# Performance work log

Hardware: AMD Instinct MI355X
Metric: run time of the kernel (lower is better)

Reference implementation:

```python
import jax, jax.numpy as jnp
import numpy as np

def setup_inputs() -> dict:
    key = jax.random.key(0)
    k1, k2 = jax.random.split(key)
    B, T_enc, T_dec, D = 8, 2048, 2048, 512
    encoder_outputs = jax.random.normal(k1, (B, T_enc, D), dtype=jnp.float32)
    decoder_outputs = jax.random.normal(k2, (B, T_dec, D), dtype=jnp.float32)
    return {"encoder_outputs": encoder_outputs, "decoder_outputs": decoder_outputs}

def reference(encoder_outputs, decoder_outputs):
    # score[b,e,t] = sum_d enc[b,e,d] * dec[b,t,d]
    score = jnp.einsum('bed,btd->bet', encoder_outputs, decoder_outputs)
    # softmax over encoder-time axis (axis=-2)
    attn = jax.nn.softmax(score, axis=1)  # [B, T_enc, T_dec]
    # context[b,t,d] = sum_e enc[b,e,d] * attn[b,e,t]  (avoids 4D broadcast)
    context = jnp.einsum('bed,bet->btd', encoder_outputs, attn)
    return jnp.concatenate([decoder_outputs, context], axis=-1)  # [B, T_dec, 2D]
```

## Files before the change

### kernel.cpp

```cpp
#include <hip/hip_runtime.h>


typedef _Float16 f16;
typedef f16 f16x8 __attribute__((ext_vector_type(8)));
typedef f16 f16x4 __attribute__((ext_vector_type(4)));
typedef float f32x4 __attribute__((ext_vector_type(4)));

#define NB 8
#define TE 2048
#define TD 2048
#define DD 512
#define TBLK 64
#define EBLK 32
#define NCH (TE / EBLK)

#define OKHI 0
#define OKT  32768
#define OS4  73728
#define OP   92160
#define OPSZ 5120
#define OAL  102400
#define OLL  102912
#define OFLG 103168
#define SMEM_BYTES 103232

__device__ __forceinline__ int swz1k(int row, int byteInRow) {
    return row * 1024 + (byteInRow ^ ((row & 7) << 4));
}

__global__ __launch_bounds__(512, 2)
void attn_fused(const float* __restrict__ enc, const float* __restrict__ dec,
                float* __restrict__ out) {
    __shared__ __align__(16) char sm[SMEM_BYTES];
    const int tid  = threadIdx.x;
    const int b    = blockIdx.x & 7;
    const int t0   = (blockIdx.x >> 3) * TBLK;
    const int lane = tid & 63;
    const int wv   = tid >> 6;
    const int li   = lane & 15;
    const int gi   = lane >> 4;
    const int et   = wv & 1;
    const int kq   = wv >> 1;
    const float L2E = 1.44269504088896f;

    const float* encB = enc + (size_t)b * TE * DD;
    const float* decB = dec + (size_t)b * TD * DD;
    float*       outB = out + (size_t)b * TD * (2 * DD);

    const int c4 = tid & 127;
    const int rb = tid >> 7;

    f32x4 st[8];
    #pragma unroll
    for (int i = 0; i < 8; ++i)
        st[i] = *(const f32x4*)(encB + (size_t)(8 * rb + i) * DD + 4 * c4);

    f16x8 qF[4][4];
    #pragma unroll
    for (int kk = 0; kk < 4; ++kk)
        #pragma unroll
        for (int tl = 0; tl < 4; ++tl) {
            const float* qp = decB + (size_t)(t0 + 16 * tl + li) * DD
                            + 128 * kq + 32 * kk + 8 * gi;
            f32x4 q0 = *(const f32x4*)qp;
            f32x4 q1 = *(const f32x4*)(qp + 4);
            f16x8 h;
            #pragma unroll
            for (int j = 0; j < 4; ++j) { h[j] = (f16)q0[j]; h[4 + j] = (f16)q1[j]; }
            qF[kk][tl] = h;
        }

    f16x4 hvB[8];
    #pragma unroll
    for (int i = 0; i < 8; ++i) {
        f16x4 h4 = {(f16)st[i][0], (f16)st[i][1], (f16)st[i][2], (f16)st[i][3]};
        hvB[i] = h4;
        *(f16x4*)(sm + OKHI + swz1k(8 * rb + i, 8 * c4)) = h4;
    }
    #pragma unroll
    for (int i = 0; i < 8; ++i)
        st[i] = *(const f32x4*)(encB + (size_t)(EBLK + 8 * rb + i) * DD + 4 * c4);
    __syncthreads();

    const int cq   = lane & 7;
    const int erq  = lane >> 3;
    const int tcol = 8 * wv + cq;
    float mrun = -1.0e30f;
    float lpart = 0.0f;

    f32x4 ctx[4][4];
    #pragma unroll
    for (int md = 0; md < 4; ++md)
        #pragma unroll
        for (int tt = 0; tt < 4; ++tt)
            ctx[md][tt] = (f32x4){0.f, 0.f, 0.f, 0.f};

    for (int ch = 0; ch < NCH; ++ch) {
        const int pb = ch & 1;
        const int qb = pb ^ 1;
        const bool doPV = (ch > 0);
        const bool more = (ch + 1 < NCH);

        f32x4 sacc[4];
        #pragma unroll
        for (int tl = 0; tl < 4; ++tl)
            sacc[tl] = (f32x4){0.f, 0.f, 0.f, 0.f};
        __builtin_amdgcn_s_setprio(1);
        #pragma unroll
        for (int kk = 0; kk < 4; ++kk) {
            int cb = 256 * kq + 64 * kk + 16 * gi;
            f16x8 aF = *(const f16x8*)(sm + OKHI + swz1k(16 * et + li, cb));
            #pragma unroll
            for (int tl = 0; tl < 4; ++tl)
                sacc[tl] = __builtin_amdgcn_mfma_f32_16x16x32_f16(aF, qF[kk][tl], sacc[tl], 0, 0, 0);
        }
        __builtin_amdgcn_s_setprio(0);
        #pragma unroll
        for (int tl = 0; tl < 4; ++tl) {
            f16x4 sh = {(f16)sacc[tl][0], (f16)sacc[tl][1],
                        (f16)sacc[tl][2], (f16)sacc[tl][3]};
            *(f16x4*)(sm + OS4 + kq * 4608 + (16 * tl + li) * 72
                      + 32 * et + 8 * gi) = sh;
        }
        __syncthreads();

        f32x4 s4 = (f32x4){0.f, 0.f, 0.f, 0.f};
        #pragma unroll
        for (int bu = 0; bu < 4; ++bu) {
            f16x4 h = *(const f16x4*)(sm + OS4 + bu * 4608 + tcol * 72 + 8 * erq);
            #pragma unroll
            for (int j = 0; j < 4; ++j) s4[j] += (float)h[j];
        }

        bool doR = false;
        f16x8 bP[4];
        if (doPV) {
            const uint4* fp = (const uint4*)(sm + OFLG + 32 * qb);
            uint4 f0 = fp[0], f1 = fp[1];
            doR = (f0.x | f0.y | f0.z | f0.w | f1.x | f1.y | f1.z | f1.w) != 0;
            #pragma unroll
            for (int tt = 0; tt < 4; ++tt)
                bP[tt] = *(const f16x8*)(sm + OP + OPSZ * qb + (16 * tt + li) * 80 + 16 * gi);
        }
        {
            float pml = fmaxf(fmaxf(s4[0], s4[1]), fmaxf(s4[2], s4[3]));
            bool trip = pml > mrun + 8.0f;
            unsigned long long bal = __ballot(trip);
            float alpha = 1.0f;
            if (bal != 0ULL) {
                float pm = pml;
                pm = fmaxf(pm, __shfl_xor(pm, 8));
                pm = fmaxf(pm, __shfl_xor(pm, 16));
                pm = fmaxf(pm, __shfl_xor(pm, 32));
                float mnew = fmaxf(mrun, pm);
                alpha = exp2f((mrun - mnew) * L2E);
                lpart *= alpha;
                mrun = mnew;
            }
            f32x4 p4;
            #pragma unroll
            for (int j = 0; j < 4; ++j) p4[j] = exp2f((s4[j] - mrun) * L2E);
            lpart += p4[0] + p4[1] + p4[2] + p4[3];
            f16x4 pw = {(f16)p4[0], (f16)p4[1], (f16)p4[2], (f16)p4[3]};
            *(f16x4*)(sm + OP + OPSZ * pb + tcol * 80 + 8 * erq) = pw;
            if (erq == 0) *(float*)(sm + OAL + 256 * pb + 4 * tcol) = alpha;
            if (lane == 0) *(unsigned*)(sm + OFLG + 32 * pb + 4 * wv) = (bal != 0ULL) ? 1u : 0u;
        }
        if (doPV) {
            if (doR) {
                float av[4];
                #pragma unroll
                for (int tt = 0; tt < 4; ++tt)
                    av[tt] = *(const float*)(sm + OAL + 256 * qb + 4 * (16 * tt + li));
                #pragma unroll
                for (int md = 0; md < 4; ++md)
                    #pragma unroll
                    for (int tt = 0; tt < 4; ++tt)
                        #pragma unroll
                        for (int r = 0; r < 4; ++r) ctx[md][tt][r] *= av[tt];
            }
            __builtin_amdgcn_s_setprio(1);
            #pragma unroll
            for (int md = 0; md < 4; ++md) {
                int dv = 64 * wv + 16 * md + li;
                int sig = ((dv >> 3) & 3) << 4;
                f16x8 a = *(const f16x8*)(sm + OKT + dv * 80 + ((16 * gi) ^ sig));
                #pragma unroll
                for (int tt = 0; tt < 4; ++tt)
                    ctx[md][tt] = __builtin_amdgcn_mfma_f32_16x16x32_f16(a, bP[tt], ctx[md][tt], 0, 0, 0);
            }
            __builtin_amdgcn_s_setprio(0);
        }
        f16x4 hvA[8];
        if (more) {
            #pragma unroll
            for (int i = 0; i < 8; ++i) {
                f16x4 h4 = {(f16)st[i][0], (f16)st[i][1], (f16)st[i][2], (f16)st[i][3]};
                hvA[i] = h4;
                *(f16x4*)(sm + OKHI + swz1k(8 * rb + i, 8 * c4)) = h4;
            }
            if (ch + 2 < NCH) {
                const float* src = encB + (size_t)(ch + 2) * EBLK * DD;
                #pragma unroll
                for (int i = 0; i < 8; ++i)
                    st[i] = *(const f32x4*)(src + (size_t)(8 * rb + i) * DD + 4 * c4);
            }
        }
        __syncthreads();
        #pragma unroll
        for (int k = 0; k < 4; ++k) {
            int d = 4 * c4 + k;
            int sig = ((d >> 3) & 3) << 4;
            f16x8 q8 = {hvB[0][k], hvB[1][k], hvB[2][k], hvB[3][k],
                        hvB[4][k], hvB[5][k], hvB[6][k], hvB[7][k]};
            *(f16x8*)(sm + OKT + d * 80 + ((16 * rb) ^ sig)) = q8;
        }
        if (more) {
            #pragma unroll
            for (int i = 0; i < 8; ++i) hvB[i] = hvA[i];
        }
    }

    __syncthreads();

    {
        const int qb2 = (NCH - 1) & 1;
        const uint4* fp = (const uint4*)(sm + OFLG + 32 * qb2);
        uint4 f0 = fp[0], f1 = fp[1];
        bool doR = (f0.x | f0.y | f0.z | f0.w | f1.x | f1.y | f1.z | f1.w) != 0;
        f16x8 bP[4];
        #pragma unroll
        for (int tt = 0; tt < 4; ++tt)
            bP[tt] = *(const f16x8*)(sm + OP + OPSZ * qb2 + (16 * tt + li) * 80 + 16 * gi);
        if (doR) {
            float av[4];
            #pragma unroll
            for (int tt = 0; tt < 4; ++tt)
                av[tt] = *(const float*)(sm + OAL + 256 * qb2 + 4 * (16 * tt + li));
            #pragma unroll
            for (int md = 0; md < 4; ++md)
                #pragma unroll
                for (int tt = 0; tt < 4; ++tt)
                    #pragma unroll
                    for (int r = 0; r < 4; ++r) ctx[md][tt][r] *= av[tt];
        }
        #pragma unroll
        for (int md = 0; md < 4; ++md) {
            int dv = 64 * wv + 16 * md + li;
            int sig = ((dv >> 3) & 3) << 4;
            f16x8 a = *(const f16x8*)(sm + OKT + dv * 80 + ((16 * gi) ^ sig));
            #pragma unroll
            for (int tt = 0; tt < 4; ++tt)
                ctx[md][tt] = __builtin_amdgcn_mfma_f32_16x16x32_f16(a, bP[tt], ctx[md][tt], 0, 0, 0);
        }
    }

    {
        float ps = lpart;
        ps += __shfl_xor(ps, 8);
        ps += __shfl_xor(ps, 16);
        ps += __shfl_xor(ps, 32);
        if (erq == 0) *(float*)(sm + OLL + 4 * tcol) = ps;
    }
    __syncthreads();
    float inv[4];
    #pragma unroll
    for (int tt = 0; tt < 4; ++tt)
        inv[tt] = 1.0f / *(const float*)(sm + OLL + 4 * (16 * tt + li));
    #pragma unroll
    for (int md = 0; md < 4; ++md)
        #pragma unroll
        for (int tt = 0; tt < 4; ++tt) {
            int t = t0 + 16 * tt + li;
            int d = 64 * wv + 16 * md + 4 * gi;
            float4 o;
            o.x = ctx[md][tt][0] * inv[tt];
            o.y = ctx[md][tt][1] * inv[tt];
            o.z = ctx[md][tt][2] * inv[tt];
            o.w = ctx[md][tt][3] * inv[tt];
            *(float4*)(outB + (size_t)t * (2 * DD) + DD + d) = o;
        }
    #pragma unroll
    for (int it = 0; it < TBLK * (DD / 4) / 512; ++it) {
        int i = tid + it * 512;
        int t = i >> 7, cc = i & 127;
        float4 q = ((const float4*)(decB + (size_t)(t0 + t) * DD))[cc];
        ((float4*)(outB + (size_t)(t0 + t) * (2 * DD)))[cc] = q;
    }
}

extern "C" void kernel_launch(void* const* d_in, const int* in_sizes, int n_in,
                              void* d_out, int out_size, void* d_ws, size_t ws_size,
                              hipStream_t stream) {
    const float* enc = (const float*)d_in[0];
    const float* dec = (const float*)d_in[1];
    float* out = (float*)d_out;
    dim3 grid(NB * (TD / TBLK));
    dim3 block(512);
    attn_fused<<<grid, block, 0, stream>>>(enc, dec, out);
}
```

Measured before the change: 132.9 us.

## Software-pipeline softmax of previous chunk against current chunk's QK MFMAs

Double-buffers the shared-memory score staging area. Each iteration now reduces and exponentiates the scores of the previous chunk while the QK^T MFMAs for the current chunk run, instead of waiting on a barrier between the score write and the softmax. The last chunk's softmax and PV move into a longer epilogue with an extra barrier. LDS use grows by about 18 KB, which may reduce occupancy and adds register pressure from the prefetched score fragments.

```diff
diff --git a/kernel.cpp b/kernel.cpp
--- a/kernel.cpp
+++ b/kernel.cpp
@@ -17,12 +17,13 @@
 #define OKHI 0
 #define OKT  32768
 #define OS4  73728
-#define OP   92160
+#define OS4SZ 18432
+#define OP   110592
 #define OPSZ 5120
-#define OAL  102400
-#define OLL  102912
-#define OFLG 103168
-#define SMEM_BYTES 103232
+#define OAL  120832
+#define OLL  121344
+#define OFLG 121600
+#define SMEM_BYTES 121664
 
 __device__ __forceinline__ int swz1k(int row, int byteInRow) {
     return row * 1024 + (byteInRow ^ ((row & 7) << 4));
@@ -97,10 +98,16 @@
 
     for (int ch = 0; ch < NCH; ++ch) {
         const int pb = ch & 1;
-        const int qb = pb ^ 1;
-        const bool doPV = (ch > 0);
+        const int sp = (ch + 1) & 1;
+        const bool doSM = (ch > 0);
         const bool more = (ch + 1 < NCH);
 
+        f16x4 sh4[4];
+        if (doSM) {
+            #pragma unroll
+            for (int bu = 0; bu < 4; ++bu)
+                sh4[bu] = *(const f16x4*)(sm + OS4 + OS4SZ * sp + bu * 4608 + tcol * 72 + 8 * erq);
+        }
         f32x4 sacc[4];
         #pragma unroll
         for (int tl = 0; tl < 4; ++tl)
@@ -115,34 +122,12 @@
                 sacc[tl] = __builtin_amdgcn_mfma_f32_16x16x32_f16(aF, qF[kk][tl], sacc[tl], 0, 0, 0);
         }
         __builtin_amdgcn_s_setprio(0);
-        #pragma unroll
-        for (int tl = 0; tl < 4; ++tl) {
-            f16x4 sh = {(f16)sacc[tl][0], (f16)sacc[tl][1],
-                        (f16)sacc[tl][2], (f16)sacc[tl][3]};
-            *(f16x4*)(sm + OS4 + kq * 4608 + (16 * tl + li) * 72
-                      + 32 * et + 8 * gi) = sh;
-        }
-        __syncthreads();
-
-        f32x4 s4 = (f32x4){0.f, 0.f, 0.f, 0.f};
-        #pragma unroll
-        for (int bu = 0; bu < 4; ++bu) {
-            f16x4 h = *(const f16x4*)(sm + OS4 + bu * 4608 + tcol * 72 + 8 * erq);
-            #pragma unroll
-            for (int j = 0; j < 4; ++j) s4[j] += (float)h[j];
-        }
-
-        bool doR = false;
-        f16x8 bP[4];
-        if (doPV) {
-            const uint4* fp = (const uint4*)(sm + OFLG + 32 * qb);
-            uint4 f0 = fp[0], f1 = fp[1];
-            doR = (f0.x | f0.y | f0.z | f0.w | f1.x | f1.y | f1.z | f1.w) != 0;
-            #pragma unroll
-            for (int tt = 0; tt < 4; ++tt)
-                bP[tt] = *(const f16x8*)(sm + OP + OPSZ * qb + (16 * tt + li) * 80 + 16 * gi);
-        }
-        {
+        if (doSM) {
+            f32x4 s4 = (f32x4){0.f, 0.f, 0.f, 0.f};
+            #pragma unroll
+            for (int bu = 0; bu < 4; ++bu)
+                #pragma unroll
+                for (int j = 0; j < 4; ++j) s4[j] += (float)sh4[bu][j];
             float pml = fmaxf(fmaxf(s4[0], s4[1]), fmaxf(s4[2], s4[3]));
             bool trip = pml > mrun + 8.0f;
             unsigned long long bal = __ballot(trip);
@@ -162,16 +147,32 @@
             for (int j = 0; j < 4; ++j) p4[j] = exp2f((s4[j] - mrun) * L2E);
             lpart += p4[0] + p4[1] + p4[2] + p4[3];
             f16x4 pw = {(f16)p4[0], (f16)p4[1], (f16)p4[2], (f16)p4[3]};
-            *(f16x4*)(sm + OP + OPSZ * pb + tcol * 80 + 8 * erq) = pw;
-            if (erq == 0) *(float*)(sm + OAL + 256 * pb + 4 * tcol) = alpha;
-            if (lane == 0) *(unsigned*)(sm + OFLG + 32 * pb + 4 * wv) = (bal != 0ULL) ? 1u : 0u;
-        }
-        if (doPV) {
+            *(f16x4*)(sm + OP + OPSZ * sp + tcol * 80 + 8 * erq) = pw;
+            if (erq == 0) *(float*)(sm + OAL + 256 * sp + 4 * tcol) = alpha;
+            if (lane == 0) *(unsigned*)(sm + OFLG + 32 * sp + 4 * wv) = (bal != 0ULL) ? 1u : 0u;
+        }
+        #pragma unroll
+        for (int tl = 0; tl < 4; ++tl) {
+            f16x4 sh = {(f16)sacc[tl][0], (f16)sacc[tl][1],
+                        (f16)sacc[tl][2], (f16)sacc[tl][3]};
+            *(f16x4*)(sm + OS4 + OS4SZ * pb + kq * 4608 + (16 * tl + li) * 72
+                      + 32 * et + 8 * gi) = sh;
+        }
+        __syncthreads();
+
+        if (doSM) {
+            const uint4* fp = (const uint4*)(sm + OFLG + 32 * sp);
+            uint4 f0 = fp[0], f1 = fp[1];
+            bool doR = (f0.x | f0.y | f0.z | f0.w | f1.x | f1.y | f1.z | f1.w) != 0;
+            f16x8 bP[4];
+            #pragma unroll
+            for (int tt = 0; tt < 4; ++tt)
+                bP[tt] = *(const f16x8*)(sm + OP + OPSZ * sp + (16 * tt + li) * 80 + 16 * gi);
             if (doR) {
                 float av[4];
                 #pragma unroll
                 for (int tt = 0; tt < 4; ++tt)
-                    av[tt] = *(const float*)(sm + OAL + 256 * qb + 4 * (16 * tt + li));
+                    av[tt] = *(const float*)(sm + OAL + 256 * sp + 4 * (16 * tt + li));
                 #pragma unroll
                 for (int md = 0; md < 4; ++md)
                     #pragma unroll
@@ -224,19 +225,53 @@
     __syncthreads();
 
     {
-        const int qb2 = (NCH - 1) & 1;
-        const uint4* fp = (const uint4*)(sm + OFLG + 32 * qb2);
+        const int sp2 = (NCH - 1) & 1;
+        f32x4 s4 = (f32x4){0.f, 0.f, 0.f, 0.f};
+        #pragma unroll
+        for (int bu = 0; bu < 4; ++bu) {
+            f16x4 h = *(const f16x4*)(sm + OS4 + OS4SZ * sp2 + bu * 4608 + tcol * 72 + 8 * erq);
+            #pragma unroll
+            for (int j = 0; j < 4; ++j) s4[j] += (float)h[j];
+        }
+        float pml = fmaxf(fmaxf(s4[0], s4[1]), fmaxf(s4[2], s4[3]));
+        bool trip = pml > mrun + 8.0f;
+        unsigned long long bal = __ballot(trip);
+        float alpha = 1.0f;
+        if (bal != 0ULL) {
+            float pm = pml;
+            pm = fmaxf(pm, __shfl_xor(pm, 8));
+            pm = fmaxf(pm, __shfl_xor(pm, 16));
+            pm = fmaxf(pm, __shfl_xor(pm, 32));
+            float mnew = fmaxf(mrun, pm);
+            alpha = exp2f((mrun - mnew) * L2E);
+            lpart *= alpha;
+            mrun = mnew;
+        }
+        f32x4 p4;
+        #pragma unroll
+        for (int j = 0; j < 4; ++j) p4[j] = exp2f((s4[j] - mrun) * L2E);
+        lpart += p4[0] + p4[1] + p4[2] + p4[3];
+        f16x4 pw = {(f16)p4[0], (f16)p4[1], (f16)p4[2], (f16)p4[3]};
+        *(f16x4*)(sm + OP + OPSZ * sp2 + tcol * 80 + 8 * erq) = pw;
+        if (erq == 0) *(float*)(sm + OAL + 256 * sp2 + 4 * tcol) = alpha;
+        if (lane == 0) *(unsigned*)(sm + OFLG + 32 * sp2 + 4 * wv) = (bal != 0ULL) ? 1u : 0u;
+    }
+    __syncthreads();
+
+    {
+        const int sp2 = (NCH - 1) & 1;
+        const uint4* fp = (const uint4*)(sm + OFLG + 32 * sp2);
         uint4 f0 = fp[0], f1 = fp[1];
         bool doR = (f0.x | f0.y | f0.z | f0.w | f1.x | f1.y | f1.z | f1.w) != 0;
         f16x8 bP[4];
         #pragma unroll
         for (int tt = 0; tt < 4; ++tt)
-            bP[tt] = *(const f16x8*)(sm + OP + OPSZ * qb2 + (16 * tt + li) * 80 + 16 * gi);
+            bP[tt] = *(const f16x8*)(sm + OP + OPSZ * sp2 + (16 * tt + li) * 80 + 16 * gi);
         if (doR) {
             float av[4];
             #pragma unroll
             for (int tt = 0; tt < 4; ++tt)
-                av[tt] = *(const float*)(sm + OAL + 256 * qb2 + 4 * (16 * tt + li));
+                av[tt] = *(const float*)(sm + OAL + 256 * sp2 + 4 * (16 * tt + li));
             #pragma unroll
             for (int md = 0; md < 4; ++md)
                 #pragma unroll
```

Result: slower. 153.1 us (+15.2%).
